# Performance work log

Hardware: AMD Instinct MI355X
Metric: run time of the kernel (lower is better)

Reference implementation:

```python
import jax, jax.numpy as jnp
import numpy as np

B, D, H, C = 8192, 1024, 128, 16


def setup_inputs() -> dict:
    key = jax.random.key(0)
    ks = jax.random.split(key, 6)
    x = jax.random.normal(ks[0], (B, D), dtype=jnp.float32)
    c = jax.random.randint(ks[1], (B,), 0, C, dtype=jnp.int32)
    # per-condition 2-layer MLP params (fc1: D->H, fc2: H->D), torch Linear layout [out,in]
    W1 = jax.random.normal(ks[2], (C, H, D), dtype=jnp.float32) * 0.02
    b1 = jax.random.normal(ks[3], (C, H), dtype=jnp.float32) * 0.02
    W2 = jax.random.normal(ks[4], (C, D, H), dtype=jnp.float32) * 0.02
    b2 = jax.random.normal(ks[5], (C, D), dtype=jnp.float32) * 0.02
    return {"x": x, "c": c, "W1": W1, "b1": b1, "W2": W2, "b2": b2}


def reference(x, c, W1, b1, W2, b2):
    # embeddingnet treated as identity: embedded_x = x  [B, D]
    # Hard condition routing: compute every condition's mini-MLP densely, then
    # select the row matching each sample's condition (jit-friendly grouped GEMM).
    h_all = jnp.einsum('bd,chd->cbh', x, W1) + b1[:, None, :]          # [C, B, H]
    out_all = jnp.einsum('cbh,cdh->cbd', h_all, W2) + b2[:, None, :]   # [C, B, D]
    masked = out_all[c, jnp.arange(x.shape[0])]                        # [B, D]
    # l2_embed = True branch
    norm = jnp.linalg.norm(masked, axis=1, keepdims=True) + 1e-10
    masked = masked / norm
    mask_norm = jnp.float32(0.0)
    embed_norm = jnp.linalg.norm(x)
    return (masked, mask_norm, embed_norm, x)
```

## Files before the change

kernel.cpp:

```cpp
#include <hip/hip_runtime.h>
#include <hip/hip_bf16.h>
#include <math.h>

#define B_ 8192
#define D_ 1024
#define H_ 128
#define C_ 16
#define BD (B_*D_)
#define SUBR 16
#define SLOTS 68
#define MAXSUB 150
#define GRID_F (8 * SLOTS)

using bf16x8 = __attribute__((ext_vector_type(8))) __bf16;
using f32x4  = __attribute__((ext_vector_type(4))) float;
typedef unsigned short ushort_t;


__device__ inline bf16x8 cvt8(float4 a, float4 b) {
    bf16x8 r;
    r[0] = (__bf16)a.x; r[1] = (__bf16)a.y; r[2] = (__bf16)a.z; r[3] = (__bf16)a.w;
    r[4] = (__bf16)b.x; r[5] = (__bf16)b.y; r[6] = (__bf16)b.z; r[7] = (__bf16)b.w;
    return r;
}
__device__ inline unsigned pack2(float a, float b) {
    unsigned ua = __builtin_bit_cast(unsigned short, (__bf16)a);
    unsigned ub = __builtin_bit_cast(unsigned short, (__bf16)b);
    return ua | (ub << 16);
}

__global__ __launch_bounds__(256) void k_prep(const float* __restrict__ W1f,
                                              const float* __restrict__ W2f,
                                              const int* __restrict__ c,
                                              __bf16* __restrict__ w1s,
                                              __bf16* __restrict__ w2s,
                                              int* __restrict__ w,
                                              float* __restrict__ ep) {
    int bid = blockIdx.x, tid = threadIdx.x;
    if (bid < 128) {
#pragma unroll
        for (int u = 0; u < 8; ++u) {
            int g = bid * 2048 + u * 256 + tid;
            int cond = g >> 14, jf = (g >> 11) & 7, ks = (g >> 6) & 31, lam = g & 63;
            int l15 = lam & 15, kg = lam >> 4;
            const float* src = W1f + ((size_t)cond * 128 + jf * 16 + l15) * 1024 + ks * 32 + kg * 8;
            *(bf16x8*)(w1s + (size_t)g * 8) = cvt8(*(const float4*)src, *(const float4*)(src + 4));
        }
    } else if (bid < 256) {
        int wb = bid - 128;
#pragma unroll
        for (int u = 0; u < 8; ++u) {
            int g = wb * 2048 + u * 256 + tid;
            int cond = g >> 14, jf = (g >> 8) & 63, ks = (g >> 6) & 3, lam = g & 63;
            int l15 = lam & 15, kg = lam >> 4;
            const float* src = W2f + ((size_t)cond * 1024 + jf * 16 + l15) * 128 + ks * 32 + kg * 8;
            *(bf16x8*)(w2s + (size_t)g * 8) = cvt8(*(const float4*)src, *(const float4*)(src + 4));
        }
    } else {
        __shared__ int hist[C_], base[C_], poff[C_], nt[C_];
        if (tid < C_) { hist[tid] = 0; ep[tid] = 0.0f; }
        if (tid == 0) w[24] = 0;
        __syncthreads();
        for (int i = tid; i < B_; i += 256) atomicAdd(&hist[c[i]], 1);
        __syncthreads();
        if (tid == 0) {
            int off = 0;
            for (int cc = 0; cc < C_; ++cc) {
                nt[cc] = (hist[cc] + SUBR - 1) >> 4;
                poff[cc] = off;
                base[cc] = off;
                off += nt[cc] * SUBR;
            }
        }
        __syncthreads();
        if (tid < C_) {
            int cc = tid, xcd = cc >> 1;
            int s0 = (cc & 1) ? nt[cc - 1] : 0;
            int end = poff[cc] + hist[cc];
            for (int t = 0; t < nt[cc]; ++t) {
                int* e = &w[32 + (xcd * MAXSUB + s0 + t) * 3];
                e[0] = cc; e[1] = poff[cc] + t * SUBR; e[2] = end;
            }
            if ((cc & 1) == 0) w[16 + xcd] = nt[cc] + nt[cc + 1];
        }
        __syncthreads();
        for (int i = tid; i < B_; i += 256) {
            int pos = atomicAdd(&base[c[i]], 1);
            w[8192 + pos] = i;
        }
    }
}

__global__ __launch_bounds__(512, 4) void k_f(const float* __restrict__ x,
                                              const __bf16* __restrict__ w1s,
                                              const __bf16* __restrict__ w2s,
                                              const float* __restrict__ b1f,
                                              const float* __restrict__ b2f,
                                              int* __restrict__ wsi,
                                              float* __restrict__ out,
                                              float* __restrict__ ep) {
    int xcd = blockIdx.x & 7, slot0 = blockIdx.x >> 3;
    int nsub = wsi[16 + xcd];
    const int* sidx = wsi + 8192;

    __shared__ ulong2 xot_raw[2048];
    __shared__ ushort_t Hs[16 * 128];
    __shared__ float sqs[16 * 8];
    char* ldsx = (char*)xot_raw;
    unsigned* Ot32 = (unsigned*)xot_raw;

    int tid = threadIdx.x, wv = tid >> 6, lane = tid & 63, l15 = lane & 15, kg = lane >> 4;
    int sr = wv * 2 + (lane >> 5);
    int cg = lane & 31;
    int skg = cg & 3, skb = cg >> 2;
    float xsq = 0.0f;

    for (int si = slot0; si < nsub; si += SLOTS) {
        const int* e = wsi + 32 + (xcd * MAXSUB + si) * 3;
        int cond = e[0], prow0 = e[1], end = e[2];

        {
            int pr = prow0 + sr;
            bool valid = pr < end;
            int orow = sidx[valid ? pr : (end - 1)];
            const float* xs = x + (size_t)orow * D_;
            float* xc = out + (size_t)BD + 2 + (size_t)orow * D_;
#pragma unroll 1
            for (int it = 0; it < 4; ++it) {
                int col0 = it * 256 + cg * 8;
                float4 f0 = *(const float4*)(xs + col0);
                float4 f1 = *(const float4*)(xs + col0 + 4);
                int ks = it * 8 + skb;
                *(bf16x8*)(ldsx + ks * 1024 + skg * 256 + ((sr ^ skb) * 16)) = cvt8(f0, f1);
                if (valid) {
                    float2* xo = (float2*)(xc + col0);
                    xo[0] = make_float2(f0.x, f0.y); xo[1] = make_float2(f0.z, f0.w);
                    xo[2] = make_float2(f1.x, f1.y); xo[3] = make_float2(f1.z, f1.w);
                    xsq += f0.x*f0.x + f0.y*f0.y + f0.z*f0.z + f0.w*f0.w
                         + f1.x*f1.x + f1.y*f1.y + f1.z*f1.z + f1.w*f1.w;
                }
            }
        }
        __syncthreads();

        const char* bA = (const char*)w1s + (size_t)cond * 262144 + wv * 32768 + lane * 16;
        f32x4 acc = {};
#pragma unroll 1
        for (int kb = 0; kb < 4; ++kb) {
            bf16x8 b0 = *(const bf16x8*)(bA + (kb * 8 + 0) * 1024);
            bf16x8 b1 = *(const bf16x8*)(bA + (kb * 8 + 1) * 1024);
            bf16x8 b2 = *(const bf16x8*)(bA + (kb * 8 + 2) * 1024);
            bf16x8 b3 = *(const bf16x8*)(bA + (kb * 8 + 3) * 1024);
            bf16x8 b4 = *(const bf16x8*)(bA + (kb * 8 + 4) * 1024);
            bf16x8 b5 = *(const bf16x8*)(bA + (kb * 8 + 5) * 1024);
            bf16x8 b6 = *(const bf16x8*)(bA + (kb * 8 + 6) * 1024);
            bf16x8 b7 = *(const bf16x8*)(bA + (kb * 8 + 7) * 1024);
#pragma unroll
            for (int j = 0; j < 8; ++j) {
                int ks = kb * 8 + j;
                bf16x8 x0 = *(const bf16x8*)(ldsx + ks * 1024 + kg * 256 + ((l15 ^ (ks & 7)) * 16));
                bf16x8 bj = j == 0 ? b0 : j == 1 ? b1 : j == 2 ? b2 : j == 3 ? b3
                          : j == 4 ? b4 : j == 5 ? b5 : j == 6 ? b6 : b7;
                acc = __builtin_amdgcn_mfma_f32_16x16x32_bf16(x0, bj, acc, 0, 0, 0);
            }
        }
        __syncthreads();

        {
            int j0 = wv * 16 + l15;
            float bias = b1f[cond * 128 + j0];
            int sl0 = j0 >> 3, jb = j0 & 7;
#pragma unroll
            for (int v = 0; v < 4; ++v) {
                int r0 = kg * 4 + v;
                __bf16 h0 = (__bf16)(acc[v] + bias);
                Hs[r0 * 128 + ((sl0 ^ (r0 & 7)) * 8) + jb] = __builtin_bit_cast(ushort_t, h0);
            }
        }
        __syncthreads();

        bf16x8 pa[4];
#pragma unroll
        for (int i = 0; i < 4; ++i)
            pa[i] = *(const bf16x8*)(Hs + l15 * 128 + (((i * 4 + kg) ^ (l15 & 7)) * 8));

        const char* w2b = (const char*)w2s + (size_t)cond * 262144 + wv * 32768 + lane * 16;
        float sq[4] = {0.f, 0.f, 0.f, 0.f};
        unsigned cswz = (unsigned)((kg & 1) << 4);
#pragma unroll 1
        for (int f = 0; f < 8; ++f) {
            const char* wb = w2b + f * 4096;
            bf16x8 q0 = *(const bf16x8*)(wb);
            bf16x8 q1 = *(const bf16x8*)(wb + 1024);
            bf16x8 q2 = *(const bf16x8*)(wb + 2048);
            bf16x8 q3 = *(const bf16x8*)(wb + 3072);
            f32x4 c0 = {};
            c0 = __builtin_amdgcn_mfma_f32_16x16x32_bf16(pa[0], q0, c0, 0, 0, 0);
            c0 = __builtin_amdgcn_mfma_f32_16x16x32_bf16(pa[1], q1, c0, 0, 0, 0);
            c0 = __builtin_amdgcn_mfma_f32_16x16x32_bf16(pa[2], q2, c0, 0, 0, 0);
            c0 = __builtin_amdgcn_mfma_f32_16x16x32_bf16(pa[3], q3, c0, 0, 0, 0);
            int jg = (wv * 8 + f) * 16 + l15;
            float bias = b2f[cond * 1024 + jg];
            float t0 = c0[0] + bias, t1 = c0[1] + bias, t2 = c0[2] + bias, t3 = c0[3] + bias;
            sq[0] += t0*t0; sq[1] += t1*t1; sq[2] += t2*t2; sq[3] += t3*t3;
            unsigned jc = (unsigned)jg ^ cswz;
            Ot32[(kg * 2    ) * 1024 + jc] = pack2(t0, t1);
            Ot32[(kg * 2 + 1) * 1024 + jc] = pack2(t2, t3);
        }
#pragma unroll
        for (int v = 0; v < 4; ++v) {
            float s = sq[v];
            s += __shfl_xor(s, 1); s += __shfl_xor(s, 2);
            s += __shfl_xor(s, 4); s += __shfl_xor(s, 8);
            if (l15 == 0) sqs[(kg * 4 + v) * 8 + wv] = s;
        }
        __syncthreads();

#pragma unroll 1
        for (int rr = 0; rr < 2; ++rr) {
            int r = wv * 2 + rr;
            int pr = prow0 + r;
            if (pr < end) {
                int orow = sidx[pr];
                float s = sqs[r*8+0] + sqs[r*8+1] + sqs[r*8+2] + sqs[r*8+3]
                        + sqs[r*8+4] + sqs[r*8+5] + sqs[r*8+6] + sqs[r*8+7];
                float inv = 1.0f / (sqrtf(s) + 1e-10f);
                int hi = (r & 1) * 16;
                unsigned rswz = (unsigned)(((r >> 2) & 1) << 4);
                const unsigned* base = Ot32 + (r >> 1) * 1024;
                float4* go = (float4*)(out + (size_t)orow * D_);
#pragma unroll
                for (int it = 0; it < 4; ++it) {
                    unsigned cu = (unsigned)(lane * 4 + it * 256) ^ rswz;
                    uint4 u = *(const uint4*)(base + cu);
                    float4 v;
                    v.x = (float)__builtin_bit_cast(__bf16, (ushort_t)(u.x >> hi)) * inv;
                    v.y = (float)__builtin_bit_cast(__bf16, (ushort_t)(u.y >> hi)) * inv;
                    v.z = (float)__builtin_bit_cast(__bf16, (ushort_t)(u.z >> hi)) * inv;
                    v.w = (float)__builtin_bit_cast(__bf16, (ushort_t)(u.w >> hi)) * inv;
                    go[lane + it * 64] = v;
                }
            }
        }
        __syncthreads();
    }

    float s = xsq;
    s += __shfl_xor(s, 1);  s += __shfl_xor(s, 2);  s += __shfl_xor(s, 4);
    s += __shfl_xor(s, 8);  s += __shfl_xor(s, 16); s += __shfl_xor(s, 32);
    if (lane == 0) sqs[wv] = s;
    __syncthreads();
    if (tid == 0) {
        float t = sqs[0] + sqs[1] + sqs[2] + sqs[3] + sqs[4] + sqs[5] + sqs[6] + sqs[7];
        atomicAdd(&ep[blockIdx.x & 15], t);
        __threadfence();
        int prev = atomicAdd(&wsi[24], 1);
        if (prev == GRID_F - 1) {
            __threadfence();
            float e = 0.0f;
#pragma unroll
            for (int i = 0; i < 16; ++i) e += ep[i];
            out[BD] = 0.0f;
            out[BD + 1] = sqrtf(e);
        }
    }
}

extern "C" void kernel_launch(void* const* d_in, const int* in_sizes, int n_in,
                              void* d_out, int out_size, void* d_ws, size_t ws_size,
                              hipStream_t stream) {
    const float* x  = (const float*)d_in[0];
    const int*   c  = (const int*)d_in[1];
    const float* W1 = (const float*)d_in[2];
    const float* b1 = (const float*)d_in[3];
    const float* W2 = (const float*)d_in[4];
    const float* b2 = (const float*)d_in[5];
    float* out = (float*)d_out;
    char* ws = (char*)d_ws;
    int* wsi = (int*)ws;
    float* ep   = (float*)(ws + 131072);
    __bf16* w1s = (__bf16*)(ws + 262144);
    __bf16* w2s = (__bf16*)(ws + 4456448);

    k_prep<<<257, 256, 0, stream>>>(W1, W2, c, w1s, w2s, wsi, ep);
    k_f<<<GRID_F, 512, 0, stream>>>(x, w1s, w2s, b1, b2, wsi, out, ep);
}
```

Baseline: 77.95 us.

## Move x bf16 conversion, copy and norm reduction into prep kernel

The prep kernel gains 512 extra blocks that stream x once in contiguous order. They write a bf16 copy to workspace, write the fp32 passthrough copy of x to the output, and record per-block sums of squares. The main kernel now gathers half-size bf16 rows instead of fp32 rows, and one block reduces the partial sums into the embed norm. This replaces the atomic counter and last-block finalisation. The cost is an extra 16 MB bf16 write plus read round-trip through memory, in exchange for a lighter gather phase and no atomics in the fused kernel.

```diff
diff --git a/kernel.cpp b/kernel.cpp
--- a/kernel.cpp
+++ b/kernel.cpp
@@ -32,10 +32,13 @@
 __global__ __launch_bounds__(256) void k_prep(const float* __restrict__ W1f,
                                               const float* __restrict__ W2f,
                                               const int* __restrict__ c,
+                                              const float* __restrict__ x,
                                               __bf16* __restrict__ w1s,
                                               __bf16* __restrict__ w2s,
+                                              __bf16* __restrict__ xbf,
                                               int* __restrict__ w,
-                                              float* __restrict__ ep) {
+                                              float* __restrict__ xpart,
+                                              float* __restrict__ out) {
     int bid = blockIdx.x, tid = threadIdx.x;
     if (bid < 128) {
 #pragma unroll
@@ -56,10 +59,9 @@
             const float* src = W2f + ((size_t)cond * 1024 + jf * 16 + l15) * 128 + ks * 32 + kg * 8;
             *(bf16x8*)(w2s + (size_t)g * 8) = cvt8(*(const float4*)src, *(const float4*)(src + 4));
         }
-    } else {
+    } else if (bid == 256) {
         __shared__ int hist[C_], base[C_], poff[C_], nt[C_];
-        if (tid < C_) { hist[tid] = 0; ep[tid] = 0.0f; }
-        if (tid == 0) w[24] = 0;
+        if (tid < C_) hist[tid] = 0;
         __syncthreads();
         for (int i = tid; i < B_; i += 256) atomicAdd(&hist[c[i]], 1);
         __syncthreads();
@@ -88,17 +90,42 @@
             int pos = atomicAdd(&base[c[i]], 1);
             w[8192 + pos] = i;
         }
+    } else {
+        int xb = bid - 257;
+        size_t base0 = (size_t)xb * 16384;
+        float xsq = 0.0f;
+        float2* xo_base = (float2*)(out + (size_t)BD + 2);
+#pragma unroll 4
+        for (int u = 0; u < 8; ++u) {
+            size_t idx = base0 + u * 2048 + tid * 8;
+            float4 f0 = *(const float4*)(x + idx);
+            float4 f1 = *(const float4*)(x + idx + 4);
+            *(bf16x8*)(xbf + idx) = cvt8(f0, f1);
+            float2* xo = xo_base + (idx >> 1);
+            xo[0] = make_float2(f0.x, f0.y); xo[1] = make_float2(f0.z, f0.w);
+            xo[2] = make_float2(f1.x, f1.y); xo[3] = make_float2(f1.z, f1.w);
+            xsq += f0.x*f0.x + f0.y*f0.y + f0.z*f0.z + f0.w*f0.w
+                 + f1.x*f1.x + f1.y*f1.y + f1.z*f1.z + f1.w*f1.w;
+        }
+        float s = xsq;
+        s += __shfl_xor(s, 1);  s += __shfl_xor(s, 2);  s += __shfl_xor(s, 4);
+        s += __shfl_xor(s, 8);  s += __shfl_xor(s, 16); s += __shfl_xor(s, 32);
+        __shared__ float red[4];
+        int lane = tid & 63, wv = tid >> 6;
+        if (lane == 0) red[wv] = s;
+        __syncthreads();
+        if (tid == 0) xpart[xb] = red[0] + red[1] + red[2] + red[3];
     }
 }
 
-__global__ __launch_bounds__(512, 4) void k_f(const float* __restrict__ x,
+__global__ __launch_bounds__(512, 4) void k_f(const __bf16* __restrict__ xbf,
                                               const __bf16* __restrict__ w1s,
                                               const __bf16* __restrict__ w2s,
                                               const float* __restrict__ b1f,
                                               const float* __restrict__ b2f,
-                                              int* __restrict__ wsi,
-                                              float* __restrict__ out,
-                                              float* __restrict__ ep) {
+                                              const int* __restrict__ wsi,
+                                              const float* __restrict__ xpart,
+                                              float* __restrict__ out) {
     int xcd = blockIdx.x & 7, slot0 = blockIdx.x >> 3;
     int nsub = wsi[16 + xcd];
     const int* sidx = wsi + 8192;
@@ -113,7 +140,20 @@
     int sr = wv * 2 + (lane >> 5);
     int cg = lane & 31;
     int skg = cg & 3, skb = cg >> 2;
-    float xsq = 0.0f;
+
+    if (blockIdx.x == GRID_F - 1) {
+        float v = xpart[tid];
+        v += __shfl_xor(v, 1);  v += __shfl_xor(v, 2);  v += __shfl_xor(v, 4);
+        v += __shfl_xor(v, 8);  v += __shfl_xor(v, 16); v += __shfl_xor(v, 32);
+        if (lane == 0) sqs[wv] = v;
+        __syncthreads();
+        if (tid == 0) {
+            float e = sqs[0] + sqs[1] + sqs[2] + sqs[3] + sqs[4] + sqs[5] + sqs[6] + sqs[7];
+            out[BD] = 0.0f;
+            out[BD + 1] = sqrtf(e);
+        }
+        __syncthreads();
+    }
 
     for (int si = slot0; si < nsub; si += SLOTS) {
         const int* e = wsi + 32 + (xcd * MAXSUB + si) * 3;
@@ -121,24 +161,14 @@
 
         {
             int pr = prow0 + sr;
-            bool valid = pr < end;
-            int orow = sidx[valid ? pr : (end - 1)];
-            const float* xs = x + (size_t)orow * D_;
-            float* xc = out + (size_t)BD + 2 + (size_t)orow * D_;
-#pragma unroll 1
+            int orow = sidx[pr < end ? pr : (end - 1)];
+            const char* xs = (const char*)xbf + (size_t)orow * 2048;
+#pragma unroll
             for (int it = 0; it < 4; ++it) {
-                int col0 = it * 256 + cg * 8;
-                float4 f0 = *(const float4*)(xs + col0);
-                float4 f1 = *(const float4*)(xs + col0 + 4);
+                int m = it * 32 + cg;
+                bf16x8 v = *(const bf16x8*)(xs + m * 16);
                 int ks = it * 8 + skb;
-                *(bf16x8*)(ldsx + ks * 1024 + skg * 256 + ((sr ^ skb) * 16)) = cvt8(f0, f1);
-                if (valid) {
-                    float2* xo = (float2*)(xc + col0);
-                    xo[0] = make_float2(f0.x, f0.y); xo[1] = make_float2(f0.z, f0.w);
-                    xo[2] = make_float2(f1.x, f1.y); xo[3] = make_float2(f1.z, f1.w);
-                    xsq += f0.x*f0.x + f0.y*f0.y + f0.z*f0.z + f0.w*f0.w
-                         + f1.x*f1.x + f1.y*f1.y + f1.z*f1.z + f1.w*f1.w;
-                }
+                *(bf16x8*)(ldsx + ks * 1024 + skg * 256 + ((sr ^ skb) * 16)) = v;
             }
         }
         __syncthreads();
@@ -244,26 +274,6 @@
         }
         __syncthreads();
     }
-
-    float s = xsq;
-    s += __shfl_xor(s, 1);  s += __shfl_xor(s, 2);  s += __shfl_xor(s, 4);
-    s += __shfl_xor(s, 8);  s += __shfl_xor(s, 16); s += __shfl_xor(s, 32);
-    if (lane == 0) sqs[wv] = s;
-    __syncthreads();
-    if (tid == 0) {
-        float t = sqs[0] + sqs[1] + sqs[2] + sqs[3] + sqs[4] + sqs[5] + sqs[6] + sqs[7];
-        atomicAdd(&ep[blockIdx.x & 15], t);
-        __threadfence();
-        int prev = atomicAdd(&wsi[24], 1);
-        if (prev == GRID_F - 1) {
-            __threadfence();
-            float e = 0.0f;
-#pragma unroll
-            for (int i = 0; i < 16; ++i) e += ep[i];
-            out[BD] = 0.0f;
-            out[BD + 1] = sqrtf(e);
-        }
-    }
 }
 
 extern "C" void kernel_launch(void* const* d_in, const int* in_sizes, int n_in,
@@ -278,10 +288,11 @@
     float* out = (float*)d_out;
     char* ws = (char*)d_ws;
     int* wsi = (int*)ws;
-    float* ep   = (float*)(ws + 131072);
-    __bf16* w1s = (__bf16*)(ws + 262144);
-    __bf16* w2s = (__bf16*)(ws + 4456448);
-
-    k_prep<<<257, 256, 0, stream>>>(W1, W2, c, w1s, w2s, wsi, ep);
-    k_f<<<GRID_F, 512, 0, stream>>>(x, w1s, w2s, b1, b2, wsi, out, ep);
-}
+    float* xpart = (float*)(ws + 131072);
+    __bf16* w1s  = (__bf16*)(ws + 262144);
+    __bf16* w2s  = (__bf16*)(ws + 4456448);
+    __bf16* xbf  = (__bf16*)(ws + 8650752);
+
+    k_prep<<<769, 256, 0, stream>>>(W1, W2, c, x, w1s, w2s, xbf, wsi, xpart, out);
+    k_f<<<GRID_F, 512, 0, stream>>>(xbf, w1s, w2s, b1, b2, wsi, xpart, out);
+}
```

New measurement: 66.03 us. 1.18x faster.
